# Kernel optimization log

Measured on AMD Instinct MI355X. Metric: run time of the kernel, lower is better.

## Reference

```python
import jax, jax.numpy as jnp
import numpy as np

EPS = 1e-8
SUCCESS_THRESHOLD = 0.7


def setup_inputs() -> dict:
    key = jax.random.key(0)
    k1, k2, k3, k4 = jax.random.split(key, 4)
    B, N, D = 256, 500000, 128
    return {
        "query": jax.random.normal(k1, (B, D), dtype=jnp.float32),
        "episode_keys": jax.random.normal(k2, (N, D), dtype=jnp.float32),
        "episode_values": jax.random.normal(k3, (N, 2 * D), dtype=jnp.float32),
        "episode_success_rates": jax.random.uniform(k4, (N,), dtype=jnp.float32),
        "top_k": 32,
    }


def reference(query, episode_keys, episode_values, episode_success_rates, top_k):
    # Cosine similarity (torch F.cosine_similarity clamps norms to eps)
    qn = query / jnp.maximum(jnp.linalg.norm(query, axis=-1, keepdims=True), EPS)
    kn = episode_keys / jnp.maximum(jnp.linalg.norm(episode_keys, axis=-1, keepdims=True), EPS)
    similarities = jnp.einsum("bd,nd->bn", qn, kn)  # [B, N]

    # Success masking; fall back to all-ones if nothing passes the threshold
    valid = episode_success_rates >= SUCCESS_THRESHOLD  # [N]
    valid = valid | ~jnp.any(valid)
    masked = similarities * valid.astype(similarities.dtype)

    # Top-k over episodes, then gather keys / values / success rates
    top_weights, top_indices = jax.lax.top_k(masked, top_k)  # [B, K]
    retrieved_keys = jnp.take(episode_keys, top_indices, axis=0)        # [B, K, D]
    retrieved_values = jnp.take(episode_values, top_indices, axis=0)    # [B, K, 2D]
    retrieved_success = jnp.take(episode_success_rates, top_indices, axis=0)  # [B, K]
    return retrieved_keys, retrieved_values, retrieved_success
```

## Files before the change

kernel.cpp:

```cpp
#include <hip/hip_runtime.h>
#include <hip/hip_bf16.h>
#include <math.h>


#define D      128
#define KSEL   32
#define CAP    16384
#define CPAD   16
#define THRESH 0.19f
#define EPSN   1e-8f

typedef __attribute__((ext_vector_type(8))) short bf16x8;
typedef __attribute__((ext_vector_type(4))) float f32x4;

__device__ inline unsigned short f2bf(float f) {
    unsigned int u = __float_as_uint(f);
    u += 0x7FFFu + ((u >> 16) & 1u);
    return (unsigned short)(u >> 16);
}

__global__ __launch_bounds__(256) void valid_any(
    const float* __restrict__ sr, int* __restrict__ flag, int N) {
    __shared__ int any;
    if (threadIdx.x == 0) any = 0;
    __syncthreads();
    int i = blockIdx.x * 256 + threadIdx.x;
    bool v = (i < N) && (sr[i] >= 0.7f);
    if (__ballot(v) && (threadIdx.x & 63) == 0) any = 1;
    __syncthreads();
    if (threadIdx.x == 0 && any) *(volatile int*)flag = 1;
}

__global__ __launch_bounds__(128) void prep_q(
    const float* __restrict__ query, float* __restrict__ qn,
    unsigned short* __restrict__ qnb) {
    __shared__ float red[2];
    int b = blockIdx.x, k = threadIdx.x;
    float v = query[b * D + k];
    float ss = v * v;
    #pragma unroll
    for (int m = 1; m < 64; m <<= 1) ss += __shfl_xor(ss, m);
    if ((k & 63) == 0) red[k >> 6] = ss;
    __syncthreads();
    float den = fmaxf(sqrtf(red[0] + red[1]), EPSN);
    float q = v / den;
    qn[b * D + k] = q;
    qnb[b * D + k] = f2bf(q);
}

#define KB_STRIDE 136
__global__ __launch_bounds__(256) void screen(
    const float* __restrict__ keys, const float* __restrict__ sr,
    const int* __restrict__ anyValid, float* __restrict__ nrm,
    const unsigned short* __restrict__ qnb,
    int* __restrict__ candCount, int* __restrict__ candIdx, int N, int B) {
    __shared__ unsigned short kb[64 * KB_STRIDE];
    int t = threadIdx.x;
    int n0 = blockIdx.x * 64;
    int noneValid = (*anyValid == 0);
    {
        int f4i = t & 31;
        int esub = t >> 5;
        #pragma unroll
        for (int it = 0; it < 8; ++it) {
            int e = it * 8 + esub;
            int n = n0 + e;
            float4 v = make_float4(0.f, 0.f, 0.f, 0.f);
            bool inb = (n < N);
            if (inb) v = *(const float4*)(keys + (size_t)n * D + f4i * 4);
            float ss = v.x * v.x + v.y * v.y + v.z * v.z + v.w * v.w;
            #pragma unroll
            for (int m = 1; m < 32; m <<= 1) ss += __shfl_xor(ss, m);
            float norm = fmaxf(sqrtf(ss), EPSN);
            float scale = 0.f;
            if (inb) {
                bool valid = (sr[n] >= 0.7f) || noneValid;
                if (f4i == 0) nrm[n] = valid ? norm : INFINITY;
                scale = valid ? (1.f / norm) : 0.f;
            }
            unsigned short* dst = kb + e * KB_STRIDE + f4i * 4;
            dst[0] = f2bf(v.x * scale); dst[1] = f2bf(v.y * scale);
            dst[2] = f2bf(v.z * scale); dst[3] = f2bf(v.w * scale);
        }
    }
    __syncthreads();
    int lane = t & 63, wave = t >> 6;
    int col = lane & 15, quad = lane >> 4;
    int eb = wave * 16;
    bf16x8 bfr[4];
    #pragma unroll
    for (int kk = 0; kk < 4; ++kk)
        bfr[kk] = *(const bf16x8*)(kb + (eb + col) * KB_STRIDE + kk * 32 + quad * 8);
    int eg = n0 + eb + col;
    for (int qt = 0; qt < (B >> 4); ++qt) {
        f32x4 acc = {0.f, 0.f, 0.f, 0.f};
        #pragma unroll
        for (int kk = 0; kk < 4; ++kk) {
            bf16x8 a = *(const bf16x8*)(qnb + (size_t)(qt * 16 + col) * D + kk * 32 + quad * 8);
            acc = __builtin_amdgcn_mfma_f32_16x16x32_bf16(a, bfr[kk], acc, 0, 0, 0);
        }
        #pragma unroll
        for (int r = 0; r < 4; ++r) {
            if (acc[r] >= THRESH) {
                int q = qt * 16 + quad * 4 + r;
                int pos = atomicAdd(&candCount[q * CPAD], 1);
                if (pos < CAP) candIdx[(size_t)q * CAP + pos] = eg;
            }
        }
    }
}

__global__ __launch_bounds__(256) void fallback_scan(
    const float* __restrict__ keys, const float* __restrict__ nrm,
    const float* __restrict__ qn, int* __restrict__ candCount,
    int* __restrict__ candIdx, int N) {
    int b = blockIdx.x;
    int cnt = candCount[b * CPAD];
    if (cnt >= KSEL && cnt <= CAP) return;
    __shared__ float qs[D];
    int t = threadIdx.x;
    if (t < D) qs[t] = qn[b * D + t];
    __syncthreads();
    int*   myI = candIdx + (size_t)b * CAP + t * 32;
    float* myV = (float*)(candIdx + (size_t)b * CAP + 8192) + t * 32;
    for (int j = 0; j < 32; ++j) { myV[j] = -1e30f; myI[j] = 0; }
    float minv = -1e30f; int mins = 0;
    for (int n = t; n < N; n += 256) {
        float m = nrm[n];
        const float4* kp = (const float4*)(keys + (size_t)n * D);
        float s = 0.f;
        #pragma unroll
        for (int j = 0; j < 32; ++j) {
            float4 kv = kp[j];
            s += qs[j*4+0] * (kv.x / m) + qs[j*4+1] * (kv.y / m)
               + qs[j*4+2] * (kv.z / m) + qs[j*4+3] * (kv.w / m);
        }
        if (s > minv) {
            myV[mins] = s; myI[mins] = n;
            minv = myV[0]; mins = 0;
            for (int j = 1; j < 32; ++j) {
                float v = myV[j];
                if (v < minv) { minv = v; mins = j; }
            }
        }
    }
    __syncthreads();
    if (t == 0) candCount[b * CPAD] = 256 * 32;
}

__global__ __launch_bounds__(192) void select_gather(
    const float* __restrict__ keys, const float* __restrict__ values,
    const float* __restrict__ sr, const float* __restrict__ nrm,
    const float* __restrict__ qn, const int* __restrict__ candCount,
    const int* __restrict__ candIdx,
    float* __restrict__ outK, float* __restrict__ outV,
    float* __restrict__ outS, int N) {
    __shared__ float qs[D];
    __shared__ float tv[192 * 32];
    __shared__ int   ti[192 * 32];
    __shared__ float redV[192];
    __shared__ int   redI[192];
    __shared__ int   wIdx[KSEL];
    int b = blockIdx.x, t = threadIdx.x;
    if (t < D) qs[t] = qn[b * D + t];
    float* myV = tv + t * 32;
    int*   myI = ti + t * 32;
    for (int j = 0; j < 32; ++j) { myV[j] = -1e30f; myI[j] = -1; }
    __syncthreads();
    int cnt = candCount[b * CPAD];
    if (cnt > CAP) cnt = CAP;
    float minv = -1e30f; int mins = 0;
    for (int c = t; c < cnt; c += 192) {
        int n = candIdx[(size_t)b * CAP + c];
        if ((unsigned)n >= (unsigned)N) continue;
        float m = nrm[n];
        const float4* kp = (const float4*)(keys + (size_t)n * D);
        float s = 0.f;
        #pragma unroll
        for (int j = 0; j < 32; ++j) {
            float4 kv = kp[j];
            s += qs[j*4+0] * (kv.x / m) + qs[j*4+1] * (kv.y / m)
               + qs[j*4+2] * (kv.z / m) + qs[j*4+3] * (kv.w / m);
        }
        if (s > minv) {
            myV[mins] = s; myI[mins] = n;
            minv = myV[0]; mins = 0;
            for (int j = 1; j < 32; ++j) {
                float v = myV[j];
                if (v < minv) { minv = v; mins = j; }
            }
        }
    }
    __syncthreads();
    for (int r = 0; r < KSEL; ++r) {
        float bv = -2e30f; int bi = 0x7fffffff;
        for (int j = 0; j < 32; ++j) {
            float v = myV[j]; int i = myI[j];
            if (v > bv || (v == bv && i < bi)) { bv = v; bi = i; }
        }
        redV[t] = bv; redI[t] = bi;
        __syncthreads();
        if (t < 64) {
            float v1 = redV[t + 64];  int i1 = redI[t + 64];
            if (v1 > bv || (v1 == bv && i1 < bi)) { bv = v1; bi = i1; }
            float v2 = redV[t + 128]; int i2 = redI[t + 128];
            if (v2 > bv || (v2 == bv && i2 < bi)) { bv = v2; bi = i2; }
            #pragma unroll
            for (int m = 32; m >= 1; m >>= 1) {
                float ov = __shfl_xor(bv, m); int oi = __shfl_xor(bi, m);
                if (ov > bv || (ov == bv && oi < bi)) { bv = ov; bi = oi; }
            }
            if (t == 0) wIdx[r] = bi;
        }
        __syncthreads();
        int w = wIdx[r];
        for (int j = 0; j < 32; ++j)
            if (myI[j] == w) myV[j] = -3e30f;
    }
    for (int i = t; i < KSEL * (D / 4); i += 192) {
        int r = i >> 5, f = i & 31;
        float4 v = *(const float4*)(keys + (size_t)wIdx[r] * D + f * 4);
        *(float4*)(outK + ((size_t)b * KSEL + r) * D + f * 4) = v;
    }
    for (int i = t; i < KSEL * (2 * D / 4); i += 192) {
        int r = i >> 6, f = i & 63;
        float4 v = *(const float4*)(values + (size_t)wIdx[r] * (2 * D) + f * 4);
        *(float4*)(outV + ((size_t)b * KSEL + r) * (2 * D) + f * 4) = v;
    }
    if (t < KSEL) outS[(size_t)b * KSEL + t] = sr[wIdx[t]];
}

extern "C" void kernel_launch(void* const* d_in, const int* in_sizes, int n_in,
                              void* d_out, int out_size, void* d_ws, size_t ws_size,
                              hipStream_t stream) {
    const float* query  = (const float*)d_in[0];
    const float* keys   = (const float*)d_in[1];
    const float* values = (const float*)d_in[2];
    const float* sr     = (const float*)d_in[3];
    const int B = in_sizes[0] / D;
    const int N = in_sizes[3];

    char* ws = (char*)d_ws;
    size_t off = 0;
    int* anyFlag = (int*)ws;
    int* candCnt = (int*)(ws + 64);
    off = 64 + (size_t)B * CPAD * 4 + 4032;
    float* qn = (float*)(ws + off);                 off += (size_t)B * D * 4;
    unsigned short* qnb = (unsigned short*)(ws + off); off += (size_t)B * D * 2;
    float* nrm = (float*)(ws + off);                off += (((size_t)N * 4 + 255) & ~(size_t)255);
    int* candIdx = (int*)(ws + off);                off += (size_t)B * CAP * 4;

    hipMemsetAsync(ws, 0, 64 + (size_t)B * CPAD * 4, stream);
    valid_any<<<(N + 255) / 256, 256, 0, stream>>>(sr, anyFlag, N);
    prep_q<<<B, 128, 0, stream>>>(query, qn, qnb);
    screen<<<(N + 63) / 64, 256, 0, stream>>>(keys, sr, anyFlag, nrm, qnb,
                                              candCnt, candIdx, N, B);
    fallback_scan<<<B, 256, 0, stream>>>(keys, nrm, qn, candCnt, candIdx, N);
    float* outK = (float*)d_out;
    float* outV = outK + (size_t)B * KSEL * D;
    float* outS = outV + (size_t)B * KSEL * 2 * D;
    select_gather<<<B, 192, 0, stream>>>(keys, values, sr, nrm, qn,
                                         candCnt, candIdx,
                                         outK, outV, outS, N);
}
```

Baseline: 1.356 ms.

## Score candidates cooperatively per half-wave and select top-k from shared memory

New measurement: 1.268 ms. -6.5%, faster.

```diff
diff --git a/kernel.cpp b/kernel.cpp
--- a/kernel.cpp
+++ b/kernel.cpp
@@ -5,7 +5,7 @@
 
 #define D      128
 #define KSEL   32
-#define CAP    16384
+#define CAP    4096
 #define CPAD   16
 #define THRESH 0.19f
 #define EPSN   1e-8f
@@ -65,19 +65,16 @@
         for (int it = 0; it < 8; ++it) {
             int e = it * 8 + esub;
             int n = n0 + e;
+            bool inb = (n < N);
+            bool valid = inb && ((sr[n] >= 0.7f) || noneValid);
             float4 v = make_float4(0.f, 0.f, 0.f, 0.f);
-            bool inb = (n < N);
-            if (inb) v = *(const float4*)(keys + (size_t)n * D + f4i * 4);
+            if (valid) v = *(const float4*)(keys + (size_t)n * D + f4i * 4);
             float ss = v.x * v.x + v.y * v.y + v.z * v.z + v.w * v.w;
             #pragma unroll
             for (int m = 1; m < 32; m <<= 1) ss += __shfl_xor(ss, m);
             float norm = fmaxf(sqrtf(ss), EPSN);
-            float scale = 0.f;
-            if (inb) {
-                bool valid = (sr[n] >= 0.7f) || noneValid;
-                if (f4i == 0) nrm[n] = valid ? norm : INFINITY;
-                scale = valid ? (1.f / norm) : 0.f;
-            }
+            if (inb && f4i == 0) nrm[n] = valid ? norm : INFINITY;
+            float scale = valid ? (1.f / norm) : 0.f;
             unsigned short* dst = kb + e * KB_STRIDE + f4i * 4;
             dst[0] = f2bf(v.x * scale); dst[1] = f2bf(v.y * scale);
             dst[2] = f2bf(v.z * scale); dst[3] = f2bf(v.w * scale);
@@ -110,7 +107,7 @@
     }
 }
 
-__global__ __launch_bounds__(256) void fallback_scan(
+__global__ __launch_bounds__(128) void fallback_scan(
     const float* __restrict__ keys, const float* __restrict__ nrm,
     const float* __restrict__ qn, int* __restrict__ candCount,
     int* __restrict__ candIdx, int N) {
@@ -118,14 +115,14 @@
     int cnt = candCount[b * CPAD];
     if (cnt >= KSEL && cnt <= CAP) return;
     __shared__ float qs[D];
+    __shared__ float tv[32 * 128];
+    __shared__ int   ti[32 * 128];
     int t = threadIdx.x;
-    if (t < D) qs[t] = qn[b * D + t];
-    __syncthreads();
-    int*   myI = candIdx + (size_t)b * CAP + t * 32;
-    float* myV = (float*)(candIdx + (size_t)b * CAP + 8192) + t * 32;
-    for (int j = 0; j < 32; ++j) { myV[j] = -1e30f; myI[j] = 0; }
+    qs[t] = qn[b * D + t];
+    __syncthreads();
+    for (int j = 0; j < 32; ++j) { tv[j * 128 + t] = -1e30f; ti[j * 128 + t] = 0; }
     float minv = -1e30f; int mins = 0;
-    for (int n = t; n < N; n += 256) {
+    for (int n = t; n < N; n += 128) {
         float m = nrm[n];
         const float4* kp = (const float4*)(keys + (size_t)n * D);
         float s = 0.f;
@@ -136,19 +133,21 @@
                + qs[j*4+2] * (kv.z / m) + qs[j*4+3] * (kv.w / m);
         }
         if (s > minv) {
-            myV[mins] = s; myI[mins] = n;
-            minv = myV[0]; mins = 0;
+            tv[mins * 128 + t] = s; ti[mins * 128 + t] = n;
+            minv = tv[t]; mins = 0;
             for (int j = 1; j < 32; ++j) {
-                float v = myV[j];
+                float v = tv[j * 128 + t];
                 if (v < minv) { minv = v; mins = j; }
             }
         }
     }
     __syncthreads();
-    if (t == 0) candCount[b * CPAD] = 256 * 32;
-}
-
-__global__ __launch_bounds__(192) void select_gather(
+    for (int j = 0; j < 32; ++j)
+        candIdx[(size_t)b * CAP + t * 32 + j] = ti[j * 128 + t];
+    if (t == 0) candCount[b * CPAD] = CAP;
+}
+
+__global__ __launch_bounds__(256) void select_gather(
     const float* __restrict__ keys, const float* __restrict__ values,
     const float* __restrict__ sr, const float* __restrict__ nrm,
     const float* __restrict__ qn, const int* __restrict__ candCount,
@@ -156,73 +155,61 @@
     float* __restrict__ outK, float* __restrict__ outV,
     float* __restrict__ outS, int N) {
     __shared__ float qs[D];
-    __shared__ float tv[192 * 32];
-    __shared__ int   ti[192 * 32];
-    __shared__ float redV[192];
-    __shared__ int   redI[192];
+    __shared__ float sc[CAP];
+    __shared__ int   si[CAP];
+    __shared__ float redV[4];
+    __shared__ int   redI[4], redC[4];
     __shared__ int   wIdx[KSEL];
     int b = blockIdx.x, t = threadIdx.x;
     if (t < D) qs[t] = qn[b * D + t];
-    float* myV = tv + t * 32;
-    int*   myI = ti + t * 32;
-    for (int j = 0; j < 32; ++j) { myV[j] = -1e30f; myI[j] = -1; }
     __syncthreads();
     int cnt = candCount[b * CPAD];
     if (cnt > CAP) cnt = CAP;
-    float minv = -1e30f; int mins = 0;
-    for (int c = t; c < cnt; c += 192) {
+    int hw = t >> 5, l = t & 31;
+    float4 q4 = *(const float4*)(qs + l * 4);
+    for (int c = hw; c < cnt; c += 8) {
         int n = candIdx[(size_t)b * CAP + c];
-        if ((unsigned)n >= (unsigned)N) continue;
+        if ((unsigned)n >= (unsigned)N) n = 0;
         float m = nrm[n];
-        const float4* kp = (const float4*)(keys + (size_t)n * D);
-        float s = 0.f;
-        #pragma unroll
-        for (int j = 0; j < 32; ++j) {
-            float4 kv = kp[j];
-            s += qs[j*4+0] * (kv.x / m) + qs[j*4+1] * (kv.y / m)
-               + qs[j*4+2] * (kv.z / m) + qs[j*4+3] * (kv.w / m);
-        }
-        if (s > minv) {
-            myV[mins] = s; myI[mins] = n;
-            minv = myV[0]; mins = 0;
-            for (int j = 1; j < 32; ++j) {
-                float v = myV[j];
-                if (v < minv) { minv = v; mins = j; }
-            }
-        }
+        float4 kv = *(const float4*)(keys + (size_t)n * D + l * 4);
+        float s = q4.x * (kv.x / m) + q4.y * (kv.y / m)
+                + q4.z * (kv.z / m) + q4.w * (kv.w / m);
+        #pragma unroll
+        for (int msk = 1; msk < 32; msk <<= 1) s += __shfl_xor(s, msk);
+        if (l == 0) { sc[c] = s; si[c] = n; }
     }
     __syncthreads();
     for (int r = 0; r < KSEL; ++r) {
-        float bv = -2e30f; int bi = 0x7fffffff;
-        for (int j = 0; j < 32; ++j) {
-            float v = myV[j]; int i = myI[j];
-            if (v > bv || (v == bv && i < bi)) { bv = v; bi = i; }
-        }
-        redV[t] = bv; redI[t] = bi;
+        float bv = -1e30f; int bi = 0x7fffffff, bc = -1;
+        for (int c = t; c < cnt; c += 256) {
+            float v = sc[c]; int n = si[c];
+            if (v > bv || (v == bv && n < bi)) { bv = v; bi = n; bc = c; }
+        }
+        #pragma unroll
+        for (int msk = 1; msk < 64; msk <<= 1) {
+            float ov = __shfl_xor(bv, msk);
+            int oi = __shfl_xor(bi, msk);
+            int oc = __shfl_xor(bc, msk);
+            if (ov > bv || (ov == bv && oi < bi)) { bv = ov; bi = oi; bc = oc; }
+        }
+        if ((t & 63) == 0) { redV[t >> 6] = bv; redI[t >> 6] = bi; redC[t >> 6] = bc; }
         __syncthreads();
-        if (t < 64) {
-            float v1 = redV[t + 64];  int i1 = redI[t + 64];
-            if (v1 > bv || (v1 == bv && i1 < bi)) { bv = v1; bi = i1; }
-            float v2 = redV[t + 128]; int i2 = redI[t + 128];
-            if (v2 > bv || (v2 == bv && i2 < bi)) { bv = v2; bi = i2; }
-            #pragma unroll
-            for (int m = 32; m >= 1; m >>= 1) {
-                float ov = __shfl_xor(bv, m); int oi = __shfl_xor(bi, m);
-                if (ov > bv || (ov == bv && oi < bi)) { bv = ov; bi = oi; }
-            }
-            if (t == 0) wIdx[r] = bi;
+        if (t == 0) {
+            for (int w = 1; w < 4; ++w)
+                if (redV[w] > bv || (redV[w] == bv && redI[w] < bi)) {
+                    bv = redV[w]; bi = redI[w]; bc = redC[w];
+                }
+            wIdx[r] = ((unsigned)bi < (unsigned)N) ? bi : 0;
+            if (bc >= 0) sc[bc] = -2e30f;
         }
         __syncthreads();
-        int w = wIdx[r];
-        for (int j = 0; j < 32; ++j)
-            if (myI[j] == w) myV[j] = -3e30f;
-    }
-    for (int i = t; i < KSEL * (D / 4); i += 192) {
+    }
+    for (int i = t; i < KSEL * (D / 4); i += 256) {
         int r = i >> 5, f = i & 31;
         float4 v = *(const float4*)(keys + (size_t)wIdx[r] * D + f * 4);
         *(float4*)(outK + ((size_t)b * KSEL + r) * D + f * 4) = v;
     }
-    for (int i = t; i < KSEL * (2 * D / 4); i += 192) {
+    for (int i = t; i < KSEL * (2 * D / 4); i += 256) {
         int r = i >> 6, f = i & 63;
         float4 v = *(const float4*)(values + (size_t)wIdx[r] * (2 * D) + f * 4);
         *(float4*)(outV + ((size_t)b * KSEL + r) * (2 * D) + f * 4) = v;
@@ -255,11 +242,11 @@
     prep_q<<<B, 128, 0, stream>>>(query, qn, qnb);
     screen<<<(N + 63) / 64, 256, 0, stream>>>(keys, sr, anyFlag, nrm, qnb,
                                               candCnt, candIdx, N, B);
-    fallback_scan<<<B, 256, 0, stream>>>(keys, nrm, qn, candCnt, candIdx, N);
+    fallback_scan<<<B, 128, 0, stream>>>(keys, nrm, qn, candCnt, candIdx, N);
     float* outK = (float*)d_out;
     float* outV = outK + (size_t)B * KSEL * D;
     float* outS = outV + (size_t)B * KSEL * 2 * D;
-    select_gather<<<B, 192, 0, stream>>>(keys, values, sr, nrm, qn,
+    select_gather<<<B, 256, 0, stream>>>(keys, values, sr, nrm, qn,
                                          candCnt, candIdx,
                                          outK, outV, outS, N);
 }
```
